# Kernel optimization log

Measured on AMD Instinct MI355X. Metric: run time of the kernel, lower is better.

## Reference

```python
import jax, jax.numpy as jnp
import numpy as np

B, S, D, K, R = 4, 2048, 2048, 8, 64


def setup_inputs() -> dict:
    key = jax.random.key(0)
    ks = jax.random.split(key, 7)
    x = jax.random.normal(ks[0], (B, S, D), dtype=jnp.float32)
    # low-rank expert factors: U_k (D,R), V_k (R,D), stacked over K
    U = jax.random.normal(ks[1], (K, D, R), dtype=jnp.float32) * 0.02
    V = jax.random.normal(ks[2], (K, R, D), dtype=jnp.float32) * 0.02
    # router MLP: Linear(D,D) -> ReLU -> Linear(D,K)
    W1 = jax.random.normal(ks[3], (D, D), dtype=jnp.float32) * 0.02
    b1 = jnp.zeros((D,), dtype=jnp.float32)
    W2 = jax.random.normal(ks[4], (D, K), dtype=jnp.float32) * 0.02
    b2 = jnp.zeros((K,), dtype=jnp.float32)
    return {"x": x, "U": U, "V": V, "W1": W1, "b1": b1, "W2": W2, "b2": b2}


def reference(x, U, V, W1, b1, W2, b2):
    # router: alpha = softmax(MLP(x)) over K experts
    h = jax.nn.relu(jnp.einsum('bsd,de->bse', x, W1) + b1)
    alpha = jax.nn.softmax(jnp.einsum('bse,ek->bsk', h, W2) + b2, axis=-1)  # [B,S,K]
    # T_eff @ x with T_eff = sum_k alpha_k * U_k V_k, computed in factored form
    vx = jnp.einsum('krd,bsd->bskr', V, x)       # [B,S,K,R]
    uvx = jnp.einsum('kdr,bskr->bskd', U, vx)    # [B,S,K,D]
    out = jnp.einsum('bsk,bskd->bsd', alpha, uvx)
    return out
```

## Files before the change

kernel.cpp:

```cpp
#include <hip/hip_runtime.h>

typedef unsigned short u16;
typedef unsigned int u32;
typedef __bf16 bf16x8 __attribute__((ext_vector_type(8)));
typedef float f32x4 __attribute__((ext_vector_type(4)));
typedef u16 u16x8 __attribute__((ext_vector_type(8)));

__device__ __forceinline__ u16 f2bf(float f) {
  u32 u = __builtin_bit_cast(u32, f);
  u += 0x7FFFu + ((u >> 16) & 1u);
  return (u16)(u >> 16);
}
__device__ __forceinline__ float bf2f(u16 h) {
  u32 u = ((u32)h) << 16;
  return __builtin_bit_cast(float, u);
}

#define GLD16(gp, lp)                                                      \
  __builtin_amdgcn_global_load_lds(                                        \
      (const __attribute__((address_space(1))) void*)(gp),                 \
      (__attribute__((address_space(3))) void*)(lp), 16, 0, 0)

__global__ void cvt_f32_bf16(const float* __restrict__ in, u16* __restrict__ out, int n8) {
  int i = blockIdx.x * 256 + threadIdx.x;
  if (i >= n8) return;
  const float4* p = (const float4*)in + (size_t)i * 2;
  float4 a = p[0], b = p[1];
  u16x8 o;
  o[0] = f2bf(a.x); o[1] = f2bf(a.y); o[2] = f2bf(a.z); o[3] = f2bf(a.w);
  o[4] = f2bf(b.x); o[5] = f2bf(b.y); o[6] = f2bf(b.z); o[7] = f2bf(b.w);
  *((u16x8*)out + i) = o;
}

__global__ void transpose_cvt(const float* __restrict__ W1, u16* __restrict__ W1t) {
  __shared__ float tile[32][33];
  const int tx = threadIdx.x;
  const int ty = threadIdx.y;
  const int e0 = blockIdx.x * 32, d0 = blockIdx.y * 32;
#pragma unroll
  for (int j = 0; j < 4; ++j)
    tile[ty + j * 8][tx] = W1[(size_t)(d0 + ty + j * 8) * 2048 + e0 + tx];
  __syncthreads();
#pragma unroll
  for (int j = 0; j < 4; ++j)
    W1t[(size_t)(e0 + ty + j * 8) * 2048 + d0 + tx] = f2bf(tile[tx][ty + j * 8]);
}

__global__ void make_Ut(const float* __restrict__ U, u16* __restrict__ Ut) {
  int idx = blockIdx.x * 256 + threadIdx.x;
  int n = idx >> 9;
  int kr = idx & 511;
  int k = kr >> 6, r = kr & 63;
  Ut[idx] = f2bf(U[(size_t)k * 131072 + (size_t)n * 64 + r]);
}

template <int EPI>
__launch_bounds__(256, 2)
__global__ void gemm_bt(const u16* __restrict__ A, const u16* __restrict__ Bt,
                        float* __restrict__ Cf, u16* __restrict__ Cb,
                        const float* __restrict__ bias, const float* __restrict__ alpha,
                        int M, int N, int Kd) {
  __shared__ u16 As[128 * 64];
  __shared__ u16 Bs[128 * 64];

  const int nbx = N >> 7;
  const int nwg = (M >> 7) * nbx;
  int wg = blockIdx.x;
  wg = (wg & 7) * (nwg >> 3) + (wg >> 3);
  const int bx = wg % nbx, by = wg / nbx;
  const int bm = by << 7, bn = bx << 7;

  const int tid = threadIdx.x;
  const int lane = tid & 63, wave = tid >> 6;
  const int wr = wave >> 1, wc = wave & 1;
  const int l15 = lane & 15, hi = lane >> 4;
  const int swz7 = l15 & 7;

  f32x4 acc[4][4];
#pragma unroll
  for (int m = 0; m < 4; ++m)
#pragma unroll
    for (int n = 0; n < 4; ++n)
      acc[m][n] = f32x4{0.f, 0.f, 0.f, 0.f};

  const int srow = tid >> 3;
  const int swzc = ((tid & 7) ^ (srow & 7)) << 3;
  const size_t ldsBase = (size_t)wave * 64 * 8;

  int aBase[4], bBase[4];
#pragma unroll
  for (int m = 0; m < 4; ++m) {
    aBase[m] = (wr * 64 + m * 16 + l15) * 64;
    bBase[m] = (wc * 64 + m * 16 + l15) * 64;
  }

  const u16* Ag = A + (size_t)(bm + srow) * Kd + swzc;
  const u16* Bg = Bt + (size_t)(bn + srow) * Kd + swzc;

  for (int k0 = 0; k0 < Kd; k0 += 64) {
#pragma unroll
    for (int i = 0; i < 4; ++i) {
      GLD16(Ag + (size_t)(i * 32) * Kd + k0, (u16*)As + i * 2048 + ldsBase);
      GLD16(Bg + (size_t)(i * 32) * Kd + k0, (u16*)Bs + i * 2048 + ldsBase);
    }
    __syncthreads();
#pragma unroll
    for (int kk = 0; kk < 2; ++kk) {
      const int soff = ((kk * 4 + hi) ^ swz7) << 3;
      bf16x8 av[4], bv[4];
#pragma unroll
      for (int m = 0; m < 4; ++m) av[m] = *(const bf16x8*)(As + aBase[m] + soff);
#pragma unroll
      for (int n = 0; n < 4; ++n) bv[n] = *(const bf16x8*)(Bs + bBase[n] + soff);
#pragma unroll
      for (int m = 0; m < 4; ++m)
#pragma unroll
        for (int n = 0; n < 4; ++n)
          acc[m][n] = __builtin_amdgcn_mfma_f32_16x16x32_bf16(av[m], bv[n], acc[m][n], 0, 0, 0);
    }
    __syncthreads();
  }

#pragma unroll
  for (int m = 0; m < 4; ++m) {
    const int row0 = bm + wr * 64 + m * 16 + hi * 4;
#pragma unroll
    for (int n = 0; n < 4; ++n) {
      const int col = bn + wc * 64 + n * 16 + l15;
      f32x4 v = acc[m][n];
      if (EPI == 0) {
        const float bsv = bias[col];
#pragma unroll
        for (int j = 0; j < 4; ++j) {
          float t = v[j] + bsv;
          t = t > 0.f ? t : 0.f;
          Cb[(size_t)(row0 + j) * N + col] = f2bf(t);
        }
      } else if (EPI == 1) {
        const int e = col >> 6;
#pragma unroll
        for (int j = 0; j < 4; ++j) {
          float t = v[j] * alpha[(size_t)(row0 + j) * 8 + e];
          Cb[(size_t)(row0 + j) * N + col] = f2bf(t);
        }
      } else {
#pragma unroll
        for (int j = 0; j < 4; ++j)
          Cf[(size_t)(row0 + j) * N + col] = v[j];
      }
    }
  }
}

__global__ void router(const u16* __restrict__ hb, const float* __restrict__ W2,
                       const float* __restrict__ b2, float* __restrict__ alphaOut) {
  const int row = blockIdx.x * 4 + (threadIdx.x >> 6);
  const int lane = threadIdx.x & 63;
  const u16* h = hb + (size_t)row * 2048;
  float a8[8] = {0.f, 0.f, 0.f, 0.f, 0.f, 0.f, 0.f, 0.f};
#pragma unroll
  for (int it = 0; it < 4; ++it) {
    const int d0 = it * 512 + lane * 8;
    u16x8 hv = *(const u16x8*)(h + d0);
#pragma unroll
    for (int jj = 0; jj < 8; ++jj) {
      const float hf = bf2f(hv[jj]);
      const float4* wp = (const float4*)(W2 + (size_t)(d0 + jj) * 8);
      float4 w0 = wp[0], w1 = wp[1];
      a8[0] += hf * w0.x; a8[1] += hf * w0.y; a8[2] += hf * w0.z; a8[3] += hf * w0.w;
      a8[4] += hf * w1.x; a8[5] += hf * w1.y; a8[6] += hf * w1.z; a8[7] += hf * w1.w;
    }
  }
#pragma unroll
  for (int off = 32; off; off >>= 1)
#pragma unroll
    for (int e = 0; e < 8; ++e) a8[e] += __shfl_xor(a8[e], off);
  if (lane == 0) {
    float mx = -1e30f;
#pragma unroll
    for (int e = 0; e < 8; ++e) { a8[e] += b2[e]; mx = a8[e] > mx ? a8[e] : mx; }
    float s = 0.f;
#pragma unroll
    for (int e = 0; e < 8; ++e) { a8[e] = __expf(a8[e] - mx); s += a8[e]; }
    const float inv = 1.f / s;
#pragma unroll
    for (int e = 0; e < 8; ++e) alphaOut[(size_t)row * 8 + e] = a8[e] * inv;
  }
}

extern "C" void kernel_launch(void* const* d_in, const int* in_sizes, int n_in,
                              void* d_out, int out_size, void* d_ws, size_t ws_size,
                              hipStream_t stream) {
  const float* x  = (const float*)d_in[0];
  const float* U  = (const float*)d_in[1];
  const float* V  = (const float*)d_in[2];
  const float* W1 = (const float*)d_in[3];
  const float* b1 = (const float*)d_in[4];
  const float* W2 = (const float*)d_in[5];
  const float* b2 = (const float*)d_in[6];
  float* out = (float*)d_out;

  char* w = (char*)d_ws;
  u16* xb   = (u16*)w; w += (size_t)16777216 * 2;
  u16* W1t  = (u16*)w; w += (size_t)4194304 * 2;
  u16* hb   = (u16*)w; w += (size_t)16777216 * 2;
  u16* Vb   = (u16*)w; w += (size_t)1048576 * 2;
  u16* Ut   = (u16*)w; w += (size_t)1048576 * 2;
  u16* wb   = (u16*)w; w += (size_t)4194304 * 2;
  float* alpha = (float*)w;

  cvt_f32_bf16<<<8192, 256, 0, stream>>>(x, xb, 2097152);
  cvt_f32_bf16<<<512, 256, 0, stream>>>(V, Vb, 131072);
  transpose_cvt<<<dim3(64, 64), dim3(32, 8), 0, stream>>>(W1, W1t);
  make_Ut<<<4096, 256, 0, stream>>>(U, Ut);

  gemm_bt<0><<<1024, 256, 0, stream>>>(xb, W1t, nullptr, hb, b1, nullptr, 8192, 2048, 2048);
  router<<<2048, 256, 0, stream>>>(hb, W2, b2, alpha);
  gemm_bt<1><<<256, 256, 0, stream>>>(xb, Vb, nullptr, wb, nullptr, alpha, 8192, 512, 2048);
  gemm_bt<2><<<1024, 256, 0, stream>>>(wb, Ut, out, nullptr, nullptr, nullptr, 8192, 2048, 512);
}
```

Before: 332.0 us.

## Add 256x256 double-buffered pipelined GEMM for router and up-projection

Adds a new 512-thread GEMM kernel with 256x256 output tiles, LDS double buffering and interleaved global-to-LDS staging. Explicit waitcnt, barriers and setprio bracket the MFMA phases so loads overlap compute. It replaces the 128x128 kernel for the router first layer and the final U projection, aiming at more data reuse per tile and hidden memory latency. The cost is 128 KB of LDS per block and higher register pressure, which may limit occupancy. There are only 256 workgroups per launch.

Result: no change. 336.2 us (+1.3%).

```diff
diff --git a/kernel.cpp b/kernel.cpp
--- a/kernel.cpp
+++ b/kernel.cpp
@@ -20,6 +20,18 @@
   __builtin_amdgcn_global_load_lds(                                        \
       (const __attribute__((address_space(1))) void*)(gp),                 \
       (__attribute__((address_space(3))) void*)(lp), 16, 0, 0)
+
+#define LGKM0()                                          \
+  do {                                                   \
+    asm volatile("s_waitcnt lgkmcnt(0)" ::: "memory");   \
+    __builtin_amdgcn_sched_barrier(0);                   \
+  } while (0)
+#define VMCNT(n)                                              \
+  do {                                                        \
+    asm volatile("s_waitcnt vmcnt(" #n ")" ::: "memory");     \
+    __builtin_amdgcn_sched_barrier(0);                        \
+  } while (0)
+#define BAR() __builtin_amdgcn_s_barrier()
 
 __global__ void cvt_f32_bf16(const float* __restrict__ in, u16* __restrict__ out, int n8) {
   int i = blockIdx.x * 256 + threadIdx.x;
@@ -55,6 +67,142 @@
 }
 
 template <int EPI>
+__launch_bounds__(512, 2)
+__global__ void gemm256(const u16* __restrict__ A, const u16* __restrict__ Bt,
+                        float* __restrict__ Cf, u16* __restrict__ Cb,
+                        const float* __restrict__ bias, int M, int N, int Kd) {
+  __shared__ u16 lds[2][4][8192];
+
+  const int nbx = N >> 8;
+  const int nwg = (M >> 8) * nbx;
+  int wg = blockIdx.x;
+  wg = (wg & 7) * (nwg >> 3) + (wg >> 3);
+  const int bx = wg % nbx, by = wg / nbx;
+  const int bm = by << 8, bn = bx << 8;
+
+  const int tid = threadIdx.x;
+  const int lane = tid & 63, wave = tid >> 6;
+  const int wr = wave >> 2;
+  const int wc = wave & 3;
+  const int hc = 2 + (wc >> 1);
+  const int l15 = lane & 15, hi = lane >> 4;
+  const int swz = l15 & 7;
+
+  const int scol = ((tid & 7) ^ ((tid >> 3) & 7)) << 3;
+  const size_t goff0 = (size_t)(tid >> 3) * Kd + scol;
+  const size_t goff1 = goff0 + (size_t)64 * Kd;
+  const int d0e = tid * 8, d1e = tid * 8 + 4096;
+
+  const int NT = Kd >> 6;
+
+  int aidx[8], bidx[4];
+#pragma unroll
+  for (int m = 0; m < 8; ++m) aidx[m] = (m * 16 + l15) * 64;
+#pragma unroll
+  for (int n = 0; n < 4; ++n) bidx[n] = ((wc & 1) * 64 + n * 16 + l15) * 64;
+  const int slot0 = ((0 * 4 + hi) ^ swz) << 3;
+  const int slot1 = ((1 * 4 + hi) ^ swz) << 3;
+
+  f32x4 acc[8][4];
+#pragma unroll
+  for (int m = 0; m < 8; ++m)
+#pragma unroll
+    for (int n = 0; n < 4; ++n) acc[m][n] = f32x4{0.f, 0.f, 0.f, 0.f};
+
+#define STAGE(tt, ht)                                                          \
+  do {                                                                         \
+    const u16* g_ = ((ht) < 2 ? A + (size_t)(bm + ((ht) & 1) * 128) * Kd       \
+                              : Bt + (size_t)(bn + ((ht) & 1) * 128) * Kd)     \
+                    + (size_t)(tt) * 64;                                       \
+    u16* l_ = &lds[(tt) & 1][(ht)][0];                                         \
+    GLD16(g_ + goff0, l_ + d0e);                                               \
+    GLD16(g_ + goff1, l_ + d1e);                                               \
+  } while (0)
+
+#define MFMA2(av, bv, nA, nB)                                                  \
+  _Pragma("unroll") for (int m = 0; m < 8; ++m) {                              \
+    acc[m][nA] = __builtin_amdgcn_mfma_f32_16x16x32_bf16(av[m], bv[nA], acc[m][nA], 0, 0, 0); \
+    acc[m][nB] = __builtin_amdgcn_mfma_f32_16x16x32_bf16(av[m], bv[nB], acc[m][nB], 0, 0, 0); \
+  }
+
+  STAGE(0, 0); STAGE(0, 1); STAGE(0, 2); STAGE(0, 3);
+  STAGE(1, 0); STAGE(1, 1); STAGE(1, 2);
+  VMCNT(6);
+  BAR();
+
+  for (int t = 0; t < NT; ++t) {
+    const int b = t & 1;
+    const u16* As = &lds[b][wr][0];
+    const u16* Bs = &lds[b][hc][0];
+    bf16x8 av0[8], bv0[4], av1[8], bv1[4];
+
+#pragma unroll
+    for (int m = 0; m < 8; ++m) av0[m] = *(const bf16x8*)(As + aidx[m] + slot0);
+#pragma unroll
+    for (int n = 0; n < 4; ++n) bv0[n] = *(const bf16x8*)(Bs + bidx[n] + slot0);
+    if (t + 1 < NT) STAGE(t + 1, 3);
+    BAR();
+    LGKM0();
+    __builtin_amdgcn_s_setprio(1);
+    MFMA2(av0, bv0, 0, 1);
+    __builtin_amdgcn_s_setprio(0);
+    BAR();
+
+#pragma unroll
+    for (int m = 0; m < 8; ++m) av1[m] = *(const bf16x8*)(As + aidx[m] + slot1);
+#pragma unroll
+    for (int n = 0; n < 4; ++n) bv1[n] = *(const bf16x8*)(Bs + bidx[n] + slot1);
+    BAR();
+    LGKM0();
+    __builtin_amdgcn_s_setprio(1);
+    MFMA2(av0, bv0, 2, 3);
+    __builtin_amdgcn_s_setprio(0);
+    BAR();
+
+    if (t + 2 < NT) { STAGE(t + 2, 0); STAGE(t + 2, 1); }
+    BAR();
+    __builtin_amdgcn_s_setprio(1);
+    MFMA2(av1, bv1, 0, 1);
+    __builtin_amdgcn_s_setprio(0);
+    BAR();
+
+    if (t + 2 < NT) STAGE(t + 2, 2);
+    BAR();
+    __builtin_amdgcn_s_setprio(1);
+    MFMA2(av1, bv1, 2, 3);
+    __builtin_amdgcn_s_setprio(0);
+    if (t < NT - 2) { VMCNT(6); }
+    else if (t == NT - 2) { VMCNT(0); }
+    BAR();
+  }
+#undef STAGE
+#undef MFMA2
+
+#pragma unroll
+  for (int m = 0; m < 8; ++m) {
+    const int row0 = bm + wr * 128 + m * 16 + hi * 4;
+#pragma unroll
+    for (int n = 0; n < 4; ++n) {
+      const int col = bn + wc * 64 + n * 16 + l15;
+      f32x4 v = acc[m][n];
+      if (EPI == 0) {
+        const float bsv = bias[col];
+#pragma unroll
+        for (int j = 0; j < 4; ++j) {
+          float tv = v[j] + bsv;
+          tv = tv > 0.f ? tv : 0.f;
+          Cb[(size_t)(row0 + j) * N + col] = f2bf(tv);
+        }
+      } else {
+#pragma unroll
+        for (int j = 0; j < 4; ++j)
+          Cf[(size_t)(row0 + j) * N + col] = v[j];
+      }
+    }
+  }
+}
+
+template <int EPI>
 __launch_bounds__(256, 2)
 __global__ void gemm_bt(const u16* __restrict__ A, const u16* __restrict__ Bt,
                         float* __restrict__ Cf, u16* __restrict__ Cb,
@@ -128,15 +276,7 @@
     for (int n = 0; n < 4; ++n) {
       const int col = bn + wc * 64 + n * 16 + l15;
       f32x4 v = acc[m][n];
-      if (EPI == 0) {
-        const float bsv = bias[col];
-#pragma unroll
-        for (int j = 0; j < 4; ++j) {
-          float t = v[j] + bsv;
-          t = t > 0.f ? t : 0.f;
-          Cb[(size_t)(row0 + j) * N + col] = f2bf(t);
-        }
-      } else if (EPI == 1) {
+      if (EPI == 1) {
         const int e = col >> 6;
 #pragma unroll
         for (int j = 0; j < 4; ++j) {
@@ -214,8 +354,8 @@
   transpose_cvt<<<dim3(64, 64), dim3(32, 8), 0, stream>>>(W1, W1t);
   make_Ut<<<4096, 256, 0, stream>>>(U, Ut);
 
-  gemm_bt<0><<<1024, 256, 0, stream>>>(xb, W1t, nullptr, hb, b1, nullptr, 8192, 2048, 2048);
+  gemm256<0><<<256, 512, 0, stream>>>(xb, W1t, nullptr, hb, b1, 8192, 2048, 2048);
   router<<<2048, 256, 0, stream>>>(hb, W2, b2, alpha);
   gemm_bt<1><<<256, 256, 0, stream>>>(xb, Vb, nullptr, wb, nullptr, alpha, 8192, 512, 2048);
-  gemm_bt<2><<<1024, 256, 0, stream>>>(wb, Ut, out, nullptr, nullptr, nullptr, 8192, 2048, 512);
-}
+  gemm256<2><<<256, 512, 0, stream>>>(wb, Ut, out, nullptr, nullptr, 8192, 2048, 512);
+}
```
